# Kernel optimization log

Hardware: AMD Instinct MI355X
Metric: run time of the kernel (lower is better)

Reference implementation:

```python
import jax, jax.numpy as jnp
import numpy as np

NARROW = 127.0                      # narrow int8 range [-127, 127]
ACT_SCALE = 6.0 / 127.0             # fixed stand-in for learned ActQuant per-tensor scale
FLOW_SCALE = 3.96875 / 127.0        # ConstFlowQuant: max_val 3.96875, 8-bit narrow


def ste_round(x):
    # straight-through rounding (Brevitas-style)
    return x + jax.lax.stop_gradient(jnp.round(x) - x)


def act_quant(x, scale):
    # per-tensor narrow int8 fake-quant (quantize -> clamp -> dequantize)
    return scale * jnp.clip(ste_round(x / scale), -NARROW, NARROW)


def weight_quant(w):
    # per-tensor stats-based narrow int8 weight fake-quant
    s = jax.lax.stop_gradient(jnp.max(jnp.abs(w))) / NARROW + 1e-12
    return s * jnp.clip(ste_round(w / s), -NARROW, NARROW)


def conv2d(x, w, b, groups=1, pad=0):
    y = jax.lax.conv_general_dilated(
        x, w, window_strides=(1, 1), padding=[(pad, pad), (pad, pad)],
        dimension_numbers=("NCHW", "OIHW", "NCHW"), feature_group_count=groups)
    return y + b[None, :, None, None]


def setup_inputs() -> dict:
    key = jax.random.key(0)
    ks = jax.random.split(key, 12)
    B, H, W = 8, 120, 160
    cor_planes = 4 * (2 * 3 + 1) ** 2  # 196
    return {
        "flow": jax.random.normal(ks[0], (B, 2, H, W), jnp.float32),
        "corr": jax.random.normal(ks[1], (B, cor_planes, H, W), jnp.float32),
        "Wc1": jax.random.normal(ks[2], (96, cor_planes, 1, 1), jnp.float32) * 0.05,
        "bc1": jax.random.normal(ks[3], (96,), jnp.float32) * 0.05,
        "Wf1": jax.random.normal(ks[4], (64, 2, 1, 1), jnp.float32) * 0.05,
        "bf1": jax.random.normal(ks[5], (64,), jnp.float32) * 0.05,
        "Wf2": jax.random.normal(ks[6], (32, 64, 1, 1), jnp.float32) * 0.05,
        "bf2": jax.random.normal(ks[7], (32,), jnp.float32) * 0.05,
        "Wd": jax.random.normal(ks[8], (128, 1, 3, 3), jnp.float32) * 0.05,
        "bd": jax.random.normal(ks[9], (128,), jnp.float32) * 0.05,
        "Wp": jax.random.normal(ks[10], (80, 128, 1, 1), jnp.float32) * 0.05,
        "bp": jax.random.normal(ks[11], (80,), jnp.float32) * 0.05,
    }


def reference(flow, corr, Wc1, bc1, Wf1, bf1, Wf2, bf2, Wd, bd, Wp, bp):
    # convc1: 1x1 quant conv with output ActQuant, then ReLU
    cor = jax.nn.relu(act_quant(conv2d(corr, weight_quant(Wc1), bc1), ACT_SCALE))
    # convf1: 1x1 quant conv (no output quant), ReLU
    flo = jax.nn.relu(conv2d(flow, weight_quant(Wf1), bf1))
    # convf2: input ActQuant, 1x1 conv, output quant (shared with convc1), ReLU
    flo = jax.nn.relu(act_quant(conv2d(act_quant(flo, ACT_SCALE), weight_quant(Wf2), bf2), ACT_SCALE))
    # QuantCat with ConstFlowQuant on inputs and output -> [B,128,H,W]
    cor_flo = act_quant(
        jnp.concatenate([act_quant(cor, FLOW_SCALE), act_quant(flo, FLOW_SCALE)], axis=1),
        FLOW_SCALE)
    # depthwise 3x3 quant conv (groups=128), input ActQuant
    d = conv2d(act_quant(cor_flo, ACT_SCALE), weight_quant(Wd), bd, groups=128, pad=1)
    # pointwise 1x1 quant conv, input ActQuant, ReLU
    out = jax.nn.relu(conv2d(act_quant(d, ACT_SCALE), weight_quant(Wp), bp))
    # final QuantCat(out, flow) with ConstFlowQuant -> [B,82,H,W]
    return act_quant(
        jnp.concatenate([act_quant(out, FLOW_SCALE), act_quant(flow, FLOW_SCALE)], axis=1),
        FLOW_SCALE)
```

## Files before the change

kernel.cpp:

```cpp
#include <hip/hip_runtime.h>
#include <hip/hip_bf16.h>
#include <cstddef>

#define BB   8
#define HH   120
#define WW   160
#define HW   19200
#define NPIX 153600
#define CORC 196

#define AS_  ((float)(6.0/127.0))
#define FS_  0.03125f

#define OFF_WF1 18832
#define OFF_WF2 18960
#define OFF_WD  21008
#define OFF_WPQ_US 44320
#define CFQ_BYTE_OFF 131072

typedef __attribute__((ext_vector_type(8)))  short short8;
typedef __attribute__((ext_vector_type(4)))  float f32x4;
typedef unsigned int u32;

__device__ __forceinline__ float clip127(float x) {
    return fminf(fmaxf(x, -127.f), 127.f);
}

__device__ __forceinline__ unsigned short f2bf(float x) {
    unsigned int u = __float_as_uint(x);
    unsigned int r = (u + 0x7fffu + ((u >> 16) & 1u)) >> 16;
    return (unsigned short)r;
}

__global__ __launch_bounds__(256) void quant_weights(
    const float* __restrict__ Wc1, const float* __restrict__ Wf1,
    const float* __restrict__ Wf2, const float* __restrict__ Wd,
    const float* __restrict__ Wp,  float* __restrict__ ws)
{
    __shared__ float red[256];
    const int t = blockIdx.x;
    const float* src = (t == 0) ? Wc1 : (t == 1) ? Wf1 : (t == 2) ? Wf2 : (t == 3) ? Wd : Wp;
    const int n = (t == 0) ? 18816 : (t == 1) ? 128 : (t == 2) ? 2048 : (t == 3) ? 1152 : 10240;
    const int tid = threadIdx.x;

    float m = 0.f;
    for (int i = tid; i < n; i += 256) m = fmaxf(m, fabsf(src[i]));
    red[tid] = m;
    __syncthreads();
    for (int s = 128; s > 0; s >>= 1) {
        if (tid < s) red[tid] = fmaxf(red[tid], red[tid + s]);
        __syncthreads();
    }
    const float s = red[0] / 127.0f + 1e-12f;

    if (t == 0) {
        unsigned short* bf = (unsigned short*)ws + 32;
        for (int j = tid; j < 21504; j += 256) {
            const int e    = j & 7;
            const int l    = (j >> 3) & 63;
            const int tile = j >> 9;
            const int nt   = tile % 6;
            const int kt   = tile / 6;
            const int out  = nt * 16 + (l & 15);
            const int k    = kt * 32 + ((l >> 4) << 3) + e;
            float q = 0.f;
            if (k < 196) q = clip127(rintf(Wc1[out * 196 + k] / s));
            bf[j] = f2bf(q);
        }
        if (tid == 0) ws[2] = s;
    } else if (t == 4) {
        unsigned short* bf = (unsigned short*)ws + OFF_WPQ_US;
        for (int j = tid; j < 10240; j += 256) {
            const int e    = j & 7;
            const int l    = (j >> 3) & 63;
            const int tile = j >> 9;
            const int nt   = tile % 5;
            const int kt   = tile / 5;
            const int o    = nt * 16 + (l & 15);
            const int k    = kt * 32 + ((l >> 4) << 3) + e;
            const float q  = clip127(rintf(Wp[o * 128 + k] / s));
            bf[j] = f2bf(q);
        }
        if (tid == 0) ws[1] = s;
    } else {
        for (int i = tid; i < n; i += 256) {
            const float q = clip127(rintf(src[i] / s));
            if (t == 1) {
                ws[OFF_WF1 + i] = s * q;
            } else if (t == 2) {
                int o = i / 64, c = i % 64;
                ws[OFF_WF2 + c * 32 + o] = s * q;
            } else {
                ws[OFF_WD + i] = q;
            }
        }
        if (tid == 0 && t == 3) ws[0] = s;
    }
}

#define TSTRIDE 136
__global__ __launch_bounds__(256, 3) void k1_convc1(
    const float* __restrict__ corr, const float* __restrict__ bc1,
    const float* __restrict__ ws,   signed char* __restrict__ cfq)
{
    __shared__ __align__(1024) char smem[32768];

    const int tid = threadIdx.x;
    const int w   = tid >> 6;
    const int l   = tid & 63;
    const int p0  = blockIdx.x * 128;
    const int b   = p0 / HW;
    const int hw0 = p0 % HW;
    const float* cp = corr + (size_t)b * CORC * HW + hw0;

    const short8* Bfr = (const short8*)((const unsigned short*)ws + 32);

#define STAGE(KT, BASE)                                                               \
    {   _Pragma("unroll")                                                             \
        for (int i = 0; i < 4; ++i) {                                                 \
            const int cl = w * 8 + i * 2;                                             \
            int ch = (KT) * 32 + cl + (l >> 5);                                       \
            ch = ch < CORC ? ch : (CORC - 1);                                         \
            const char* src = (const char*)cp + (size_t)ch * (HW * 4) + ((l & 31) * 16); \
            u32* dst = (u32*)(smem + (BASE) + cl * 512);                              \
            __builtin_amdgcn_global_load_lds(                                         \
                (const __attribute__((address_space(1))) u32*)src,                    \
                (__attribute__((address_space(3))) u32*)dst, 16, 0, 0);               \
        }                                                                             }

    f32x4 a00 = {0.f,0.f,0.f,0.f}, a01 = a00, a02 = a00, a03 = a00, a04 = a00, a05 = a00;
    f32x4 a10 = a00, a11 = a00, a12 = a00, a13 = a00, a14 = a00, a15 = a00;

    STAGE(0, 0)
    STAGE(1, 16384)
    __syncthreads();

    const int pixoff = (w * 32 + (l & 15)) * 4;
    const int chbase = (l >> 4) << 3;

    for (int kt = 0; kt < 7; ++kt) {
        const int base = (kt & 1) << 14;

        const short8 b0 = Bfr[(kt * 6 + 0) * 64 + l];
        const short8 b1 = Bfr[(kt * 6 + 1) * 64 + l];
        const short8 b2 = Bfr[(kt * 6 + 2) * 64 + l];
        const short8 b3 = Bfr[(kt * 6 + 3) * 64 + l];
        const short8 b4 = Bfr[(kt * 6 + 4) * 64 + l];
        const short8 b5 = Bfr[(kt * 6 + 5) * 64 + l];

        short8 h0_, l0_, h1_, l1_;
#pragma unroll
        for (int e = 0; e < 8; ++e) {
            const char* ap = smem + base + (chbase + e) * 512 + pixoff;
            const float v0 = *(const float*)ap;
            const float v1 = *(const float*)(ap + 64);
            const unsigned short h0 = f2bf(v0);
            const unsigned short h1 = f2bf(v1);
            h0_[e] = (short)h0; h1_[e] = (short)h1;
            l0_[e] = (short)f2bf(v0 - __uint_as_float((unsigned int)h0 << 16));
            l1_[e] = (short)f2bf(v1 - __uint_as_float((unsigned int)h1 << 16));
        }

#define MF(BB_, A0, A1)                                                          \
        A0 = __builtin_amdgcn_mfma_f32_16x16x32_bf16(l0_, BB_, A0, 0, 0, 0);     \
        A0 = __builtin_amdgcn_mfma_f32_16x16x32_bf16(h0_, BB_, A0, 0, 0, 0);     \
        A1 = __builtin_amdgcn_mfma_f32_16x16x32_bf16(l1_, BB_, A1, 0, 0, 0);     \
        A1 = __builtin_amdgcn_mfma_f32_16x16x32_bf16(h1_, BB_, A1, 0, 0, 0);
        MF(b0, a00, a10) MF(b1, a01, a11) MF(b2, a02, a12)
        MF(b3, a03, a13) MF(b4, a04, a14) MF(b5, a05, a15)
#undef MF

        __syncthreads();
        if (kt < 5) STAGE(kt + 2, base)
    }
#undef STAGE

    const float sc1 = ws[2];
    signed char* t8 = (signed char*)smem;

#define EPI(ACC, NT, TILE)                                                        \
    {   const int out = (NT) * 16 + (l & 15);                                     \
        const float bias = bc1[out];                                              \
        _Pragma("unroll")                                                         \
        for (int i = 0; i < 4; ++i) {                                             \
            const int prow = w * 32 + (TILE) * 16 + ((l >> 4) << 2) + i;          \
            float v  = fmaf(sc1, ACC[i], bias);                                   \
            float aq = AS_ * clip127(rintf(v / AS_));                             \
            float r  = fmaxf(aq, 0.f);                                            \
            float kk = fminf(rintf(r * 32.f), 127.f);                             \
            float cf = kk * FS_;                                                  \
            float q8 = clip127(rintf(cf / AS_));                                  \
            t8[out * TSTRIDE + prow] = (signed char)(int)q8;                      \
        }                                                                         }
    EPI(a00, 0, 0) EPI(a01, 1, 0) EPI(a02, 2, 0) EPI(a03, 3, 0) EPI(a04, 4, 0) EPI(a05, 5, 0)
    EPI(a10, 0, 1) EPI(a11, 1, 1) EPI(a12, 2, 1) EPI(a13, 3, 1) EPI(a14, 4, 1) EPI(a15, 5, 1)
#undef EPI
    __syncthreads();

#pragma unroll
    for (int r = 0; r < 12; ++r) {
        const int d   = r * 256 + tid;
        const int out = d >> 5;
        const int pd  = d & 31;
        const unsigned int v = *(const unsigned int*)(t8 + out * TSTRIDE + pd * 4);
        *(unsigned int*)(cfq + (size_t)(b * 128 + out) * HW + hw0 + pd * 4) = v;
    }
}

typedef __attribute__((ext_vector_type(16))) float f32x16;
__global__ __launch_bounds__(256) void k1_flo(
    const float* __restrict__ flow, const float* __restrict__ bf1,
    const float* __restrict__ bf2,  const float* __restrict__ ws,
    signed char* __restrict__ cfq)
{
    const int p  = blockIdx.x * 256 + threadIdx.x;
    const int b  = p / HW;
    const int hw = p % HW;

    const float f0 = flow[(size_t)(b * 2) * HW + hw];
    const float f1 = flow[(size_t)(b * 2 + 1) * HW + hw];

    f32x16 a2a, a2b;
#pragma unroll
    for (int j = 0; j < 16; ++j) { a2a[j] = 0.f; a2b[j] = 0.f; }

    for (int c = 0; c < 64; ++c) {
        const float w0 = ws[OFF_WF1 + 2 * c];
        const float w1 = ws[OFF_WF1 + 2 * c + 1];
        float v  = fmaf(f0, w0, fmaf(f1, w1, bf1[c]));
        float r  = fmaxf(v, 0.f);
        float af = AS_ * fminf(rintf(r / AS_), 127.f);
        const float* w2 = ws + OFF_WF2 + c * 32;
#pragma unroll
        for (int j = 0; j < 16; ++j) {
            a2a[j] = fmaf(af, w2[j],      a2a[j]);
            a2b[j] = fmaf(af, w2[16 + j], a2b[j]);
        }
    }

    signed char* op = cfq + (size_t)b * 128 * HW + (size_t)96 * HW + hw;
#define FLOEPI(ACC, BASE)                                                        \
    _Pragma("unroll")                                                            \
    for (int j = 0; j < 16; ++j) {                                               \
        const int o = (BASE) + j;                                                \
        float v  = ACC[j] + bf2[o];                                              \
        float aq = AS_ * clip127(rintf(v / AS_));                                \
        float r  = fmaxf(aq, 0.f);                                               \
        float kk = fminf(rintf(r * 32.f), 127.f);                                \
        float cf = kk * FS_;                                                     \
        float q8 = clip127(rintf(cf / AS_));                                     \
        op[(size_t)o * HW] = (signed char)(int)q8;                               \
    }
    FLOEPI(a2a, 0) FLOEPI(a2b, 16)
#undef FLOEPI
}

#define STG_STRIDE 44
__global__ __launch_bounds__(256) void k2_dwpw(
    const float* __restrict__ flow, const float* __restrict__ bd,
    const float* __restrict__ bp,   const float* __restrict__ ws,
    const signed char* __restrict__ cfq, float* __restrict__ out)
{
    __shared__ signed char stage[4 * 128 * STG_STRIDE];
    __shared__ unsigned short afrag[64 * 136];

    const int tid = threadIdx.x;
    const int bid = blockIdx.x;
    const int b   = bid / 300;
    const int rem = bid % 300;
    const int h0  = (rem / 5) * 2;
    const int w0  = (rem % 5) * 32;

    for (int j = tid; j < 5120; j += 256) {
        const int i   = j % 10;
        const int c   = (j / 10) % 128;
        const int row = j / 1280;
        const int h   = h0 - 1 + row;
        const int wb  = w0 - 4 + 4 * i;
        unsigned int v = 0u;
        if (h >= 0 && h < HH && wb >= 0 && wb <= WW - 4)
            v = *(const unsigned int*)(cfq + ((size_t)(b * 128 + c) * HW + (size_t)h * WW + wb));
        *(unsigned int*)(stage + (row * 128 + c) * STG_STRIDE + i * 4) = v;
    }
    __syncthreads();

    const int c0 = tid & 63;
    const int pg = tid >> 6;
    const float sd = ws[0], sp = ws[1];
    const float ASsd = AS_ * sd;

    float wd0[9], wd1[9];
#pragma unroll
    for (int t9 = 0; t9 < 9; ++t9) {
        wd0[t9] = ws[OFF_WD + c0 * 9 + t9];
        wd1[t9] = ws[OFF_WD + (c0 + 64) * 9 + t9];
    }
    const float bd0 = bd[c0], bd1 = bd[c0 + 64];

#pragma unroll
    for (int pp = 0; pp < 16; ++pp) {
        const int pix = pg * 16 + pp;
        const int r   = pix >> 5;
        const int col = pix & 31;
        float s0 = 0.f, s1 = 0.f;
#pragma unroll
        for (int dy = 0; dy < 3; ++dy) {
            const int rb = (r + dy) * 128;
            const int xb = 3 + col;
#pragma unroll
            for (int dd = 0; dd < 3; ++dd) {
                s0 = fmaf((float)stage[(rb + c0     ) * STG_STRIDE + xb + dd], wd0[dy * 3 + dd], s0);
                s1 = fmaf((float)stage[(rb + c0 + 64) * STG_STRIDE + xb + dd], wd1[dy * 3 + dd], s1);
            }
        }
        const float q0 = clip127(rintf(fmaf(ASsd, s0, bd0) / AS_));
        const float q1 = clip127(rintf(fmaf(ASsd, s1, bd1) / AS_));
        afrag[pix * 136 + c0]      = f2bf(q0);
        afrag[pix * 136 + c0 + 64] = f2bf(q1);
    }
    __syncthreads();

    const int wv = tid >> 6;
    const int l  = tid & 63;
    const unsigned short* A = afrag + (size_t)(wv * 16 + (l & 15)) * 136 + ((l >> 4) << 3);
    const short8* Bfr = (const short8*)((const unsigned short*)ws + OFF_WPQ_US);

    f32x4 pc0 = {0.f,0.f,0.f,0.f}, pc1 = pc0, pc2 = pc0, pc3 = pc0, pc4 = pc0;

#define PTSTEP(ACC, KT, NT)                                                      \
    {   short8 bq = Bfr[((KT) * 5 + (NT)) * 64 + l];                             \
        ACC = __builtin_amdgcn_mfma_f32_16x16x32_bf16(a_, bq, ACC, 0, 0, 0);     }
#pragma unroll
    for (int kt = 0; kt < 4; ++kt) {
        short8 a_ = *(const short8*)(A + kt * 32);
        PTSTEP(pc0, kt, 0) PTSTEP(pc1, kt, 1) PTSTEP(pc2, kt, 2)
        PTSTEP(pc3, kt, 3) PTSTEP(pc4, kt, 4)
    }
#undef PTSTEP

    const float ASsp = AS_ * sp;
    float* ob = out + (size_t)b * 82 * HW;

#define PEPI(ACC, NT)                                                            \
    {   const int o = (NT) * 16 + (l & 15);                                      \
        const float bias = bp[o];                                                \
        _Pragma("unroll")                                                        \
        for (int i = 0; i < 4; ++i) {                                            \
            const int pix = wv * 16 + ((l >> 4) << 2) + i;                       \
            const int hw  = (h0 + (pix >> 5)) * WW + w0 + (pix & 31);            \
            float v = fmaf(ASsp, ACC[i], bias);                                  \
            float r = fmaxf(v, 0.f);                                             \
            float k = fminf(rintf(r * 32.f), 127.f);                             \
            ob[(size_t)o * HW + hw] = k * FS_;                                   \
        }                                                                        }
    PEPI(pc0, 0) PEPI(pc1, 1) PEPI(pc2, 2) PEPI(pc3, 3) PEPI(pc4, 4)
#undef PEPI

    if (tid < 128) {
        const int ch  = tid >> 6;
        const int pix = tid & 63;
        const int hw  = (h0 + (pix >> 5)) * WW + w0 + (pix & 31);
        const float f = flow[(size_t)(b * 2 + ch) * HW + hw];
        const float k = clip127(rintf(f * 32.f));
        ob[(size_t)(80 + ch) * HW + hw] = k * FS_;
    }
}

extern "C" void kernel_launch(void* const* d_in, const int* in_sizes, int n_in,
                              void* d_out, int out_size, void* d_ws, size_t ws_size,
                              hipStream_t stream) {
    const float* flow = (const float*)d_in[0];
    const float* corr = (const float*)d_in[1];
    const float* Wc1  = (const float*)d_in[2];
    const float* bc1  = (const float*)d_in[3];
    const float* Wf1  = (const float*)d_in[4];
    const float* bf1  = (const float*)d_in[5];
    const float* Wf2  = (const float*)d_in[6];
    const float* bf2  = (const float*)d_in[7];
    const float* Wd   = (const float*)d_in[8];
    const float* bd   = (const float*)d_in[9];
    const float* Wp   = (const float*)d_in[10];
    const float* bp   = (const float*)d_in[11];

    float* ws = (float*)d_ws;
    signed char* cfq = (signed char*)d_ws + CFQ_BYTE_OFF;
    float* out = (float*)d_out;

    quant_weights<<<5, 256, 0, stream>>>(Wc1, Wf1, Wf2, Wd, Wp, ws);
    k1_convc1<<<NPIX / 128, 256, 0, stream>>>(corr, bc1, ws, cfq);
    k1_flo<<<NPIX / 256, 256, 0, stream>>>(flow, bf1, bf2, ws, cfq);
    k2_dwpw<<<2400, 256, 0, stream>>>(flow, bd, bp, ws, cfq, out);
}
```

Baseline: 163.3 us.

## Issue next-stage LDS prefetch right after reading current tile, with explicit waitcnts

Restructures the double-buffered K loop so each iteration waits only for the oldest outstanding global->LDS loads (vmcnt(4)), reads the current tile into registers, and then, after a second barrier, issues the next STAGE before doing the bf16 split and MFMAs. The goal is to let the async global loads overlap the conversion and MFMA work instead of being issued after compute behind a full __syncthreads. The loop is also fully unrolled and pinned with sched_barriers. Correctness depends on the hand-counted vmcnt matching the outstanding load count, and the fixed instruction order may limit compiler scheduling.

```diff
diff --git a/kernel.cpp b/kernel.cpp
--- a/kernel.cpp
+++ b/kernel.cpp
@@ -133,13 +133,31 @@
 
     STAGE(0, 0)
     STAGE(1, 16384)
-    __syncthreads();
 
     const int pixoff = (w * 32 + (l & 15)) * 4;
     const int chbase = (l >> 4) << 3;
 
+#pragma unroll
     for (int kt = 0; kt < 7; ++kt) {
         const int base = (kt & 1) << 14;
+
+        asm volatile("s_waitcnt vmcnt(4)" ::: "memory");
+        __builtin_amdgcn_sched_barrier(0);
+        __builtin_amdgcn_s_barrier();
+        __builtin_amdgcn_sched_barrier(0);
+
+        float v0[8], v1[8];
+#pragma unroll
+        for (int e = 0; e < 8; ++e) {
+            const char* ap = smem + base + (chbase + e) * 512 + pixoff;
+            v0[e] = *(const float*)ap;
+            v1[e] = *(const float*)(ap + 64);
+        }
+        __builtin_amdgcn_sched_barrier(0);
+        asm volatile("s_waitcnt lgkmcnt(0)" ::: "memory");
+        __builtin_amdgcn_sched_barrier(0);
+        __builtin_amdgcn_s_barrier();
+        __builtin_amdgcn_sched_barrier(0);
 
         const short8 b0 = Bfr[(kt * 6 + 0) * 64 + l];
         const short8 b1 = Bfr[(kt * 6 + 1) * 64 + l];
@@ -147,18 +165,20 @@
         const short8 b3 = Bfr[(kt * 6 + 3) * 64 + l];
         const short8 b4 = Bfr[(kt * 6 + 4) * 64 + l];
         const short8 b5 = Bfr[(kt * 6 + 5) * 64 + l];
+        __builtin_amdgcn_sched_barrier(0);
+
+        if (kt < 5) STAGE(kt + 2, base)
+        __builtin_amdgcn_sched_barrier(0);
 
         short8 h0_, l0_, h1_, l1_;
 #pragma unroll
         for (int e = 0; e < 8; ++e) {
-            const char* ap = smem + base + (chbase + e) * 512 + pixoff;
-            const float v0 = *(const float*)ap;
-            const float v1 = *(const float*)(ap + 64);
-            const unsigned short h0 = f2bf(v0);
-            const unsigned short h1 = f2bf(v1);
-            h0_[e] = (short)h0; h1_[e] = (short)h1;
-            l0_[e] = (short)f2bf(v0 - __uint_as_float((unsigned int)h0 << 16));
-            l1_[e] = (short)f2bf(v1 - __uint_as_float((unsigned int)h1 << 16));
+            const float va = v0[e], vb = v1[e];
+            const unsigned short ha = f2bf(va);
+            const unsigned short hb = f2bf(vb);
+            h0_[e] = (short)ha; h1_[e] = (short)hb;
+            l0_[e] = (short)f2bf(va - __uint_as_float((unsigned int)ha << 16));
+            l1_[e] = (short)f2bf(vb - __uint_as_float((unsigned int)hb << 16));
         }
 
 #define MF(BB_, A0, A1)                                                          \
@@ -169,9 +189,6 @@
         MF(b0, a00, a10) MF(b1, a01, a11) MF(b2, a02, a12)
         MF(b3, a03, a13) MF(b4, a04, a14) MF(b5, a05, a15)
 #undef MF
-
-        __syncthreads();
-        if (kt < 5) STAGE(kt + 2, base)
     }
 #undef STAGE
 
```

After: 158.7 us. 1.03x faster.

## Halve convc1 pixel tile, deepen LDS pipeline to five stages, split N across waves

Applied to the files above, without the earlier changes.

The corr 1x1 conv kernel now gives each block 64 pixels instead of 128 and launches twice as many blocks. It stages five of the seven K-chunks into LDS up front with explicit vmcnt waits, and hoists all B-fragment loads into registers before the main loop. Wave pairs split the 96 output channels (3 N-tiles each), and block IDs are remapped so that consecutive blocks interleave batch images. The aim is to keep more loads in flight, hide HBM latency for this memory-bound stream, and balance work across CUs. The cost is extra registers for the hoisted B fragments and more barriers per K-step, which may lower occupancy.

```diff
diff --git a/kernel.cpp b/kernel.cpp
--- a/kernel.cpp
+++ b/kernel.cpp
@@ -98,112 +98,134 @@
     }
 }
 
-#define TSTRIDE 136
+#define NSLAB 5
+#define SLAB_B 8192
+#define CSTR 256
+#define TS8  68
 __global__ __launch_bounds__(256, 3) void k1_convc1(
     const float* __restrict__ corr, const float* __restrict__ bc1,
     const float* __restrict__ ws,   signed char* __restrict__ cfq)
 {
-    __shared__ __align__(1024) char smem[32768];
-
-    const int tid = threadIdx.x;
-    const int w   = tid >> 6;
-    const int l   = tid & 63;
-    const int p0  = blockIdx.x * 128;
-    const int b   = p0 / HW;
-    const int hw0 = p0 % HW;
+    __shared__ __align__(1024) char smem[NSLAB * SLAB_B];
+
+    const int tid  = threadIdx.x;
+    const int w    = tid >> 6;
+    const int l    = tid & 63;
+    const int bid  = blockIdx.x;
+    const int wgid = (bid & 7) * 300 + (bid >> 3);
+    const int p0   = wgid * 64;
+    const int b    = p0 / HW;
+    const int hw0  = p0 % HW;
     const float* cp = corr + (size_t)b * CORC * HW + hw0;
 
     const short8* Bfr = (const short8*)((const unsigned short*)ws + 32);
-
-#define STAGE(KT, BASE)                                                               \
-    {   _Pragma("unroll")                                                             \
-        for (int i = 0; i < 4; ++i) {                                                 \
-            const int cl = w * 8 + i * 2;                                             \
-            int ch = (KT) * 32 + cl + (l >> 5);                                       \
-            ch = ch < CORC ? ch : (CORC - 1);                                         \
-            const char* src = (const char*)cp + (size_t)ch * (HW * 4) + ((l & 31) * 16); \
-            u32* dst = (u32*)(smem + (BASE) + cl * 512);                              \
+    const int nbase = (w & 1) * 3;
+
+#define DECLB(KT)                                                              \
+    const short8 b##KT##_0 = Bfr[((KT) * 6 + nbase + 0) * 64 + l];             \
+    const short8 b##KT##_1 = Bfr[((KT) * 6 + nbase + 1) * 64 + l];             \
+    const short8 b##KT##_2 = Bfr[((KT) * 6 + nbase + 2) * 64 + l];
+    DECLB(0) DECLB(1) DECLB(2) DECLB(3) DECLB(4) DECLB(5) DECLB(6)
+#undef DECLB
+    __builtin_amdgcn_sched_barrier(0);
+
+#define STAGE(KT)                                                                     \
+    {   char* dbase = smem + ((KT) % NSLAB) * SLAB_B;                                 \
+        _Pragma("unroll")                                                             \
+        for (int i = 0; i < 2; ++i) {                                                 \
+            const int cg = w * 2 + i;                            \
+            int chl = (KT) * 32 + cg * 4 + (l >> 4);                                  \
+            chl = chl < CORC ? chl : (CORC - 1);                                      \
+            const char* src = (const char*)cp + (size_t)chl * (HW * 4)                \
+                              + (l & 15) * 16;                                        \
+            u32* dst = (u32*)(dbase + cg * 1024);                                     \
             __builtin_amdgcn_global_load_lds(                                         \
                 (const __attribute__((address_space(1))) u32*)src,                    \
                 (__attribute__((address_space(3))) u32*)dst, 16, 0, 0);               \
         }                                                                             }
 
-    f32x4 a00 = {0.f,0.f,0.f,0.f}, a01 = a00, a02 = a00, a03 = a00, a04 = a00, a05 = a00;
-    f32x4 a10 = a00, a11 = a00, a12 = a00, a13 = a00, a14 = a00, a15 = a00;
-
-    STAGE(0, 0)
-    STAGE(1, 16384)
-    __syncthreads();
-
-    const int pixoff = (w * 32 + (l & 15)) * 4;
+    STAGE(0) STAGE(1) STAGE(2) STAGE(3) STAGE(4)
+
+    const int pixoff = ((w >> 1) * 32 + (l & 15)) * 4;
     const int chbase = (l >> 4) << 3;
 
-    for (int kt = 0; kt < 7; ++kt) {
-        const int base = (kt & 1) << 14;
-
-        const short8 b0 = Bfr[(kt * 6 + 0) * 64 + l];
-        const short8 b1 = Bfr[(kt * 6 + 1) * 64 + l];
-        const short8 b2 = Bfr[(kt * 6 + 2) * 64 + l];
-        const short8 b3 = Bfr[(kt * 6 + 3) * 64 + l];
-        const short8 b4 = Bfr[(kt * 6 + 4) * 64 + l];
-        const short8 b5 = Bfr[(kt * 6 + 5) * 64 + l];
-
-        short8 h0_, l0_, h1_, l1_;
-#pragma unroll
-        for (int e = 0; e < 8; ++e) {
-            const char* ap = smem + base + (chbase + e) * 512 + pixoff;
-            const float v0 = *(const float*)ap;
-            const float v1 = *(const float*)(ap + 64);
-            const unsigned short h0 = f2bf(v0);
-            const unsigned short h1 = f2bf(v1);
-            h0_[e] = (short)h0; h1_[e] = (short)h1;
-            l0_[e] = (short)f2bf(v0 - __uint_as_float((unsigned int)h0 << 16));
-            l1_[e] = (short)f2bf(v1 - __uint_as_float((unsigned int)h1 << 16));
-        }
+    f32x4 ac00 = {0.f,0.f,0.f,0.f}, ac01 = ac00, ac02 = ac00;
+    f32x4 ac10 = ac00, ac11 = ac00, ac12 = ac00;
 
 #define MF(BB_, A0, A1)                                                          \
         A0 = __builtin_amdgcn_mfma_f32_16x16x32_bf16(l0_, BB_, A0, 0, 0, 0);     \
         A0 = __builtin_amdgcn_mfma_f32_16x16x32_bf16(h0_, BB_, A0, 0, 0, 0);     \
         A1 = __builtin_amdgcn_mfma_f32_16x16x32_bf16(l1_, BB_, A1, 0, 0, 0);     \
         A1 = __builtin_amdgcn_mfma_f32_16x16x32_bf16(h1_, BB_, A1, 0, 0, 0);
-        MF(b0, a00, a10) MF(b1, a01, a11) MF(b2, a02, a12)
-        MF(b3, a03, a13) MF(b4, a04, a14) MF(b5, a05, a15)
+
+#define KSTEP(KT, WN)                                                             \
+    {   asm volatile("s_waitcnt vmcnt(" #WN ")" ::: "memory");                    \
+        __builtin_amdgcn_sched_barrier(0);                                        \
+        __builtin_amdgcn_s_barrier();                         \
+        __builtin_amdgcn_sched_barrier(0);                                        \
+        const char* abase = smem + ((KT) % NSLAB) * SLAB_B;                       \
+        float v0[8], v1[8];                                                       \
+        _Pragma("unroll")                                                         \
+        for (int e = 0; e < 8; ++e) {                                             \
+            const char* ap = abase + (chbase + e) * CSTR + pixoff;                \
+            v0[e] = *(const float*)ap;                                            \
+            v1[e] = *(const float*)(ap + 64);                                     \
+        }                                                                         \
+        __builtin_amdgcn_sched_barrier(0);                                        \
+        asm volatile("s_waitcnt lgkmcnt(0)" ::: "memory");                        \
+        __builtin_amdgcn_sched_barrier(0);                                        \
+        __builtin_amdgcn_s_barrier();                          \
+        __builtin_amdgcn_sched_barrier(0);                                        \
+        if ((KT) + NSLAB < 7) STAGE((KT) + NSLAB)                                 \
+        __builtin_amdgcn_sched_barrier(0);                                        \
+        short8 h0_, l0_, h1_, l1_;                                                \
+        _Pragma("unroll")                                                         \
+        for (int e = 0; e < 8; ++e) {                                             \
+            const float va = v0[e], vb = v1[e];                                   \
+            const unsigned short ha = f2bf(va);                                   \
+            const unsigned short hb = f2bf(vb);                                   \
+            h0_[e] = (short)ha; h1_[e] = (short)hb;                               \
+            l0_[e] = (short)f2bf(va - __uint_as_float((unsigned int)ha << 16));   \
+            l1_[e] = (short)f2bf(vb - __uint_as_float((unsigned int)hb << 16));   \
+        }                                                                         \
+        MF(b##KT##_0, ac00, ac10) MF(b##KT##_1, ac01, ac11)                       \
+        MF(b##KT##_2, ac02, ac12)                                                 }
+
+    KSTEP(0, 8) KSTEP(1, 8) KSTEP(2, 8) KSTEP(3, 6)
+    KSTEP(4, 4) KSTEP(5, 2) KSTEP(6, 0)
+#undef KSTEP
 #undef MF
-
-        __syncthreads();
-        if (kt < 5) STAGE(kt + 2, base)
-    }
 #undef STAGE
 
     const float sc1 = ws[2];
     signed char* t8 = (signed char*)smem;
 
 #define EPI(ACC, NT, TILE)                                                        \
-    {   const int out = (NT) * 16 + (l & 15);                                     \
+    {   const int out = (nbase + (NT)) * 16 + (l & 15);                           \
         const float bias = bc1[out];                                              \
         _Pragma("unroll")                                                         \
         for (int i = 0; i < 4; ++i) {                                             \
-            const int prow = w * 32 + (TILE) * 16 + ((l >> 4) << 2) + i;          \
+            const int prow = (w >> 1) * 32 + (TILE) * 16 + ((l >> 4) << 2) + i;   \
             float v  = fmaf(sc1, ACC[i], bias);                                   \
             float aq = AS_ * clip127(rintf(v / AS_));                             \
             float r  = fmaxf(aq, 0.f);                                            \
             float kk = fminf(rintf(r * 32.f), 127.f);                             \
             float cf = kk * FS_;                                                  \
             float q8 = clip127(rintf(cf / AS_));                                  \
-            t8[out * TSTRIDE + prow] = (signed char)(int)q8;                      \
+            t8[out * TS8 + prow] = (signed char)(int)q8;                          \
         }                                                                         }
-    EPI(a00, 0, 0) EPI(a01, 1, 0) EPI(a02, 2, 0) EPI(a03, 3, 0) EPI(a04, 4, 0) EPI(a05, 5, 0)
-    EPI(a10, 0, 1) EPI(a11, 1, 1) EPI(a12, 2, 1) EPI(a13, 3, 1) EPI(a14, 4, 1) EPI(a15, 5, 1)
+    EPI(ac00, 0, 0) EPI(ac01, 1, 0) EPI(ac02, 2, 0)
+    EPI(ac10, 0, 1) EPI(ac11, 1, 1) EPI(ac12, 2, 1)
 #undef EPI
     __syncthreads();
 
 #pragma unroll
-    for (int r = 0; r < 12; ++r) {
+    for (int r = 0; r < 6; ++r) {
         const int d   = r * 256 + tid;
-        const int out = d >> 5;
-        const int pd  = d & 31;
-        const unsigned int v = *(const unsigned int*)(t8 + out * TSTRIDE + pd * 4);
-        *(unsigned int*)(cfq + (size_t)(b * 128 + out) * HW + hw0 + pd * 4) = v;
+        const int out = d >> 4;
+        const int pd  = d & 15;
+        const u32 v = *(const u32*)(t8 + out * TS8 + pd * 4);
+        *(u32*)(cfq + (size_t)(b * 128 + out) * HW + hw0 + pd * 4) = v;
     }
 }
 
@@ -387,7 +409,7 @@
     float* out = (float*)d_out;
 
     quant_weights<<<5, 256, 0, stream>>>(Wc1, Wf1, Wf2, Wd, Wp, ws);
-    k1_convc1<<<NPIX / 128, 256, 0, stream>>>(corr, bc1, ws, cfq);
+    k1_convc1<<<NPIX / 64, 256, 0, stream>>>(corr, bc1, ws, cfq);
     k1_flo<<<NPIX / 256, 256, 0, stream>>>(flow, bf1, bf2, ws, cfq);
     k2_dwpw<<<2400, 256, 0, stream>>>(flow, bd, bp, ws, cfq, out);
 }
```

New measurement: 163.4 us, median of 2. No clear change (+0.1%).
